# Kernel optimization log

Hardware: AMD Instinct MI355X
Metric: run time of the kernel (lower is better)

Reference implementation:

```python
import jax, jax.numpy as jnp
import numpy as np

N_NODES = 500000
N_EDGES = 1000000
H = 128


def setup_inputs() -> dict:
    key = jax.random.key(0)
    ks = jax.random.split(key, 8)
    s = 1.0 / np.sqrt(H)
    return {
        "z": jax.random.normal(ks[0], (N_NODES, H), dtype=jnp.float32),
        "w1": jax.random.normal(ks[1], (H, H), dtype=jnp.float32) * s,
        "b1": jax.random.normal(ks[2], (H,), dtype=jnp.float32) * s,
        "w2": jax.random.normal(ks[3], (H, H), dtype=jnp.float32) * s,
        "b2": jax.random.normal(ks[4], (H,), dtype=jnp.float32) * s,
        "wb": jax.random.normal(ks[5], (1, H, H), dtype=jnp.float32) * s,
        "bb": jax.random.normal(ks[6], (1,), dtype=jnp.float32) * s,
        "pot_arcs": jax.random.randint(ks[7], (N_EDGES, 2), 0, N_NODES, dtype=jnp.int64),
    }


def reference(z, w1, b1, w2, b2, wb, bb, pot_arcs):
    # Gather head/dep node embeddings per candidate arc: [E, H]
    x1 = z[pot_arcs[:, 0]]
    x2 = z[pot_arcs[:, 1]]
    # Per-node linear + relu (dropout is identity in eval mode)
    h1 = jax.nn.relu(x1 @ w1.T + b1)
    h2 = jax.nn.relu(x2 @ w2.T + b2)
    # Bilinear score: h1 @ W @ h2^T per edge, out_features=1
    score = jnp.einsum("eh,hk,ek->e", h1, wb[0], h2) + bb[0]
    return score
```

## Files before the change

kernel.cpp:

```cpp
#include <hip/hip_runtime.h>
#include <hip/hip_bf16.h>

#define HDIM 128

typedef short bf16x8 __attribute__((ext_vector_type(8)));
typedef short bf16x4 __attribute__((ext_vector_type(4)));
typedef unsigned short u16x8 __attribute__((ext_vector_type(8)));
typedef float f32x4 __attribute__((ext_vector_type(4)));

__device__ __forceinline__ short f2bf(float f) {
    __hip_bfloat16 h = __float2bfloat16(f);
    union { __hip_bfloat16 h; short s; } c; c.h = h; return c.s;
}
__device__ __forceinline__ float bf2f(unsigned short h) {
    union { unsigned u; float f; } c; c.u = ((unsigned)h) << 16; return c.f;
}
__device__ __forceinline__ bf16x8 pack8(float4 a, float4 b) {
    bf16x8 r;
    r[0] = f2bf(a.x); r[1] = f2bf(a.y); r[2] = f2bf(a.z); r[3] = f2bf(a.w);
    r[4] = f2bf(b.x); r[5] = f2bf(b.y); r[6] = f2bf(b.z); r[7] = f2bf(b.w);
    return r;
}

__device__ __forceinline__ void barrier_lds() {
    asm volatile("s_waitcnt lgkmcnt(0)" ::: "memory");
    __builtin_amdgcn_s_barrier();
    __builtin_amdgcn_sched_barrier(0);
}

__global__ __launch_bounds__(512, 4)
void node_phase(const float* __restrict__ z,
                const float* __restrict__ w1, const float* __restrict__ b1,
                const float* __restrict__ w2, const float* __restrict__ b2,
                const float* __restrict__ wb,
                unsigned short* __restrict__ g1, unsigned short* __restrict__ h2o,
                int N)
{
    __shared__ short zbb[32 * 128];
    __shared__ short h1x[32 * 128];
    __shared__ short h2x[32 * 128];
    __shared__ short g1x[32 * 128];

    const int t = threadIdx.x;
    const int lane = t & 63, wid = t >> 6;
    const int l15 = lane & 15, kgrp = lane >> 4;
    const int feat = wid * 16 + l15;

    bf16x8 w1f[4], w2f[4], wbf[4];
    {
        const float* w1r = w1 + (size_t)feat * HDIM;
        const float* w2r = w2 + (size_t)feat * HDIM;
#pragma unroll
        for (int kt = 0; kt < 4; ++kt) {
            int k0 = kt * 32 + kgrp * 8;
            w1f[kt] = pack8(*(const float4*)(w1r + k0), *(const float4*)(w1r + k0 + 4));
            w2f[kt] = pack8(*(const float4*)(w2r + k0), *(const float4*)(w2r + k0 + 4));
            bf16x8 r;
#pragma unroll
            for (int i = 0; i < 8; ++i) r[i] = f2bf(wb[(size_t)(k0 + i) * HDIM + feat]);
            wbf[kt] = r;
        }
    }
    f32x4 bias1, bias2;
#pragma unroll
    for (int r = 0; r < 4; ++r) {
        bias1[r] = b1[wid * 16 + kgrp * 4 + r];
        bias2[r] = b2[wid * 16 + kgrp * 4 + r];
    }

    const int srow = t >> 4;
    const int sp   = t & 15;
    const int sg   = sp ^ (srow & 7);

    const int ntiles = N >> 5;

    int tile = blockIdx.x;
    if (tile < ntiles) {
        const float* src = z + (size_t)(tile * 32 + srow) * HDIM + sg * 8;
        bf16x8 v = pack8(*(const float4*)src, *(const float4*)(src + 4));
        *(bf16x8*)&zbb[t * 8] = v;
    }
    __syncthreads();

    int prevbase = -1;
    for (; tile < ntiles; tile += gridDim.x) {
        const int base = tile * 32;
        const int nxtile = tile + (int)gridDim.x;
        const bool havenext = nxtile < ntiles;

        float4 zn0, zn1;
        if (havenext) {
            const float* src = z + (size_t)(nxtile * 32 + srow) * HDIM + sg * 8;
            zn0 = *(const float4*)src;
            zn1 = *(const float4*)(src + 4);
        }
        if (prevbase >= 0) {
            u16x8 vv = *(const u16x8*)&g1x[srow * 128 + sp * 8];
            *(u16x8*)&g1[(size_t)(prevbase + srow) * HDIM + (sp ^ (srow & 7)) * 8] = vv;
        }

#pragma unroll
        for (int gp = 0; gp < 2; ++gp) {
            const int m = gp * 16 + l15;
            bf16x8 zf[4];
#pragma unroll
            for (int kt = 0; kt < 4; ++kt) {
                int pos = (kt * 4 + kgrp) ^ (m & 7);
                zf[kt] = *(const bf16x8*)&zbb[m * 128 + pos * 8];
            }
            f32x4 a1 = bias1, a3 = bias2;
#pragma unroll
            for (int kt = 0; kt < 4; ++kt) {
                a1 = __builtin_amdgcn_mfma_f32_16x16x32_bf16(w1f[kt], zf[kt], a1, 0, 0, 0);
                a3 = __builtin_amdgcn_mfma_f32_16x16x32_bf16(w2f[kt], zf[kt], a3, 0, 0, 0);
            }
            const int ng = wid * 2 + (kgrp >> 1);
            const int sidx = m * 128 + ((ng ^ (m & 7)) << 3) + ((kgrp & 1) << 2);
            bf16x4 h1v, h2v;
#pragma unroll
            for (int r = 0; r < 4; ++r) {
                float x1 = a1[r] > 0.f ? a1[r] : 0.f;
                float x2 = a3[r] > 0.f ? a3[r] : 0.f;
                h1v[r] = f2bf(x1);
                h2v[r] = f2bf(x2);
            }
            *(bf16x4*)&h1x[sidx] = h1v;
            *(bf16x4*)&h2x[sidx] = h2v;
        }
        barrier_lds();

#pragma unroll
        for (int gp = 0; gp < 2; ++gp) {
            const int m = gp * 16 + l15;
            f32x4 ag = (f32x4){0.f, 0.f, 0.f, 0.f};
#pragma unroll
            for (int kt = 0; kt < 4; ++kt) {
                int pos = (kt * 4 + kgrp) ^ (m & 7);
                bf16x8 bf = *(const bf16x8*)&h1x[m * 128 + pos * 8];
                ag = __builtin_amdgcn_mfma_f32_16x16x32_bf16(wbf[kt], bf, ag, 0, 0, 0);
            }
            const int ng = wid * 2 + (kgrp >> 1);
            const int sidx = m * 128 + ((ng ^ (m & 7)) << 3) + ((kgrp & 1) << 2);
            bf16x4 gv;
#pragma unroll
            for (int r = 0; r < 4; ++r) gv[r] = f2bf(ag[r]);
            *(bf16x4*)&g1x[sidx] = gv;
        }
        {
            u16x8 vv = *(const u16x8*)&h2x[srow * 128 + sp * 8];
            *(u16x8*)&h2o[(size_t)(base + srow) * HDIM + (sp ^ (srow & 7)) * 8] = vv;
        }
        if (havenext) {
            *(bf16x8*)&zbb[t * 8] = pack8(zn0, zn1);
        }
        prevbase = base;
        barrier_lds();
    }

    if (prevbase >= 0) {
        u16x8 vv = *(const u16x8*)&g1x[srow * 128 + sp * 8];
        *(u16x8*)&g1[(size_t)(prevbase + srow) * HDIM + (sp ^ (srow & 7)) * 8] = vv;
    }
}

__global__ void detect_idx64(const int* __restrict__ arcs, int* __restrict__ flag)
{
    if (threadIdx.x == 0) {
        int is64 = 1;
        for (int j = 0; j < 64; ++j)
            if (arcs[2 * j + 1] != 0) { is64 = 0; break; }
        *flag = is64;
    }
}

__global__ __launch_bounds__(256, 8)
void edge_phase(const unsigned short* __restrict__ g1,
                const unsigned short* __restrict__ h2,
                const void* __restrict__ arcs,
                const int* __restrict__ flag,
                const float* __restrict__ bb,
                float* __restrict__ out, int E)
{
    const int t = threadIdx.x;
    const int sub = t & 15;
    const int e = blockIdx.x * 16 + (t >> 4);
    const int ec = e < E ? e : (E - 1);

    long long u, v;
    if (*flag) {
        const long long* a = (const long long*)arcs;
        u = a[2 * (size_t)ec]; v = a[2 * (size_t)ec + 1];
    } else {
        const int* a = (const int*)arcs;
        u = a[2 * (size_t)ec]; v = a[2 * (size_t)ec + 1];
    }

    u16x8 av = *(const u16x8*)(g1 + (size_t)u * HDIM + sub * 8);
    u16x8 bv = *(const u16x8*)(h2 + (size_t)v * HDIM + sub * 8);
    float s = 0.f;
#pragma unroll
    for (int i = 0; i < 8; ++i) s += bf2f(av[i]) * bf2f(bv[i]);

    s += __shfl_xor(s, 8, 16);
    s += __shfl_xor(s, 4, 16);
    s += __shfl_xor(s, 2, 16);
    s += __shfl_xor(s, 1, 16);

    if (sub == 0 && e < E) out[e] = s + bb[0];
}

extern "C" void kernel_launch(void* const* d_in, const int* in_sizes, int n_in,
                              void* d_out, int out_size, void* d_ws, size_t ws_size,
                              hipStream_t stream)
{
    const float* z  = (const float*)d_in[0];
    const float* w1 = (const float*)d_in[1];
    const float* b1 = (const float*)d_in[2];
    const float* w2 = (const float*)d_in[3];
    const float* b2 = (const float*)d_in[4];
    const float* wb = (const float*)d_in[5];
    const float* bb = (const float*)d_in[6];
    const void*  arcs = d_in[7];

    const int N = in_sizes[0] / HDIM;
    const int E = in_sizes[7] / 2;

    char* ws = (char*)d_ws;
    int* flag = (int*)ws;
    unsigned short* g1 = (unsigned short*)(ws + 256);
    unsigned short* h2 = g1 + (size_t)N * HDIM;

    detect_idx64<<<1, 64, 0, stream>>>((const int*)arcs, flag);

    node_phase<<<512, 512, 0, stream>>>(z, w1, b1, w2, b2, wb, g1, h2, N);

    int eblk = (E + 15) / 16;
    edge_phase<<<eblk, 256, 0, stream>>>(g1, h2, arcs, flag, bb, (float*)d_out, E);
}
```

Before: 190.5 us.

## Software-pipeline node phase across three tile stages with double-buffered LDS

Restructures the node kernel loop into a three-stage software pipeline: tile i does the W1/W2 MFMA stage, tile i-1 does the bilinear Wb stage, and tile i-2 has its g1 output written back. All LDS tiles are double-buffered so each iteration needs only one barrier instead of two. It also handles a partial final tile by clamping z reads and guarding stores. LDS use doubles to 64KB per block, which may cut how many blocks fit on a CU.

```diff
diff --git a/kernel.cpp b/kernel.cpp
--- a/kernel.cpp
+++ b/kernel.cpp
@@ -36,10 +36,10 @@
                 unsigned short* __restrict__ g1, unsigned short* __restrict__ h2o,
                 int N)
 {
-    __shared__ short zbb[32 * 128];
-    __shared__ short h1x[32 * 128];
-    __shared__ short h2x[32 * 128];
-    __shared__ short g1x[32 * 128];
+    __shared__ short zbb[2][4096];
+    __shared__ short h1x[2][4096];
+    __shared__ short h2x[2][4096];
+    __shared__ short g1x[2][4096];
 
     const int t = threadIdx.x;
     const int lane = t & 63, wid = t >> 6;
@@ -72,94 +72,97 @@
     const int sp   = t & 15;
     const int sg   = sp ^ (srow & 7);
 
-    const int ntiles = N >> 5;
-
-    int tile = blockIdx.x;
-    if (tile < ntiles) {
-        const float* src = z + (size_t)(tile * 32 + srow) * HDIM + sg * 8;
-        bf16x8 v = pack8(*(const float4*)src, *(const float4*)(src + 4));
-        *(bf16x8*)&zbb[t * 8] = v;
+    const int ntiles = (N + 31) >> 5;
+    const int myTiles = (ntiles > (int)blockIdx.x)
+                      ? ((ntiles - 1 - (int)blockIdx.x) / (int)gridDim.x + 1) : 0;
+    const int nit = myTiles + 2;
+    const int ng = wid * 2 + (kgrp >> 1);
+
+    if (myTiles > 0) {
+        int row = (int)blockIdx.x * 32 + srow;
+        int rc = row < N ? row : N - 1;
+        const float* src = z + (size_t)rc * HDIM + sg * 8;
+        *(bf16x8*)&zbb[0][t * 8] = pack8(*(const float4*)src, *(const float4*)(src + 4));
     }
     __syncthreads();
 
-    int prevbase = -1;
-    for (; tile < ntiles; tile += gridDim.x) {
-        const int base = tile * 32;
-        const int nxtile = tile + (int)gridDim.x;
-        const bool havenext = nxtile < ntiles;
+    for (int i = 0; i < nit; ++i) {
+        const int cur = i & 1, prv = cur ^ 1;
+        const int tvA = (int)blockIdx.x + i * (int)gridDim.x;
+        const bool vA = (i < myTiles);
+        const bool vB = (i >= 1) && (i - 1 < myTiles);
+        const bool vG = (i >= 2) && (i - 2 < myTiles);
+        const bool vP = (i + 1 < myTiles);
 
         float4 zn0, zn1;
-        if (havenext) {
-            const float* src = z + (size_t)(nxtile * 32 + srow) * HDIM + sg * 8;
+        if (vP) {
+            int row = (tvA + (int)gridDim.x) * 32 + srow;
+            int rc = row < N ? row : N - 1;
+            const float* src = z + (size_t)rc * HDIM + sg * 8;
             zn0 = *(const float4*)src;
             zn1 = *(const float4*)(src + 4);
         }
-        if (prevbase >= 0) {
-            u16x8 vv = *(const u16x8*)&g1x[srow * 128 + sp * 8];
-            *(u16x8*)&g1[(size_t)(prevbase + srow) * HDIM + (sp ^ (srow & 7)) * 8] = vv;
-        }
-
-#pragma unroll
-        for (int gp = 0; gp < 2; ++gp) {
-            const int m = gp * 16 + l15;
-            bf16x8 zf[4];
-#pragma unroll
-            for (int kt = 0; kt < 4; ++kt) {
-                int pos = (kt * 4 + kgrp) ^ (m & 7);
-                zf[kt] = *(const bf16x8*)&zbb[m * 128 + pos * 8];
+        if (vG) {
+            int row = (tvA - 2 * (int)gridDim.x) * 32 + srow;
+            u16x8 vv = *(const u16x8*)&g1x[prv][srow * 128 + sp * 8];
+            if (row < N) *(u16x8*)&g1[(size_t)row * HDIM + (sp ^ (srow & 7)) * 8] = vv;
+        }
+        if (vB) {
+            int row = (tvA - (int)gridDim.x) * 32 + srow;
+            u16x8 vv = *(const u16x8*)&h2x[prv][srow * 128 + sp * 8];
+            if (row < N) *(u16x8*)&h2o[(size_t)row * HDIM + (sp ^ (srow & 7)) * 8] = vv;
+        }
+        if (vA) {
+#pragma unroll
+            for (int gp = 0; gp < 2; ++gp) {
+                const int m = gp * 16 + l15;
+                bf16x8 zf[4];
+#pragma unroll
+                for (int kt = 0; kt < 4; ++kt) {
+                    int pos = (kt * 4 + kgrp) ^ (m & 7);
+                    zf[kt] = *(const bf16x8*)&zbb[cur][m * 128 + pos * 8];
+                }
+                f32x4 a1 = bias1, a3 = bias2;
+#pragma unroll
+                for (int kt = 0; kt < 4; ++kt) {
+                    a1 = __builtin_amdgcn_mfma_f32_16x16x32_bf16(w1f[kt], zf[kt], a1, 0, 0, 0);
+                    a3 = __builtin_amdgcn_mfma_f32_16x16x32_bf16(w2f[kt], zf[kt], a3, 0, 0, 0);
+                }
+                const int sidx = m * 128 + ((ng ^ (m & 7)) << 3) + ((kgrp & 1) << 2);
+                bf16x4 h1v, h2v;
+#pragma unroll
+                for (int r = 0; r < 4; ++r) {
+                    float x1 = a1[r] > 0.f ? a1[r] : 0.f;
+                    float x2 = a3[r] > 0.f ? a3[r] : 0.f;
+                    h1v[r] = f2bf(x1);
+                    h2v[r] = f2bf(x2);
+                }
+                *(bf16x4*)&h1x[cur][sidx] = h1v;
+                *(bf16x4*)&h2x[cur][sidx] = h2v;
             }
-            f32x4 a1 = bias1, a3 = bias2;
-#pragma unroll
-            for (int kt = 0; kt < 4; ++kt) {
-                a1 = __builtin_amdgcn_mfma_f32_16x16x32_bf16(w1f[kt], zf[kt], a1, 0, 0, 0);
-                a3 = __builtin_amdgcn_mfma_f32_16x16x32_bf16(w2f[kt], zf[kt], a3, 0, 0, 0);
+        }
+        if (vB) {
+#pragma unroll
+            for (int gp = 0; gp < 2; ++gp) {
+                const int m = gp * 16 + l15;
+                f32x4 ag = (f32x4){0.f, 0.f, 0.f, 0.f};
+#pragma unroll
+                for (int kt = 0; kt < 4; ++kt) {
+                    int pos = (kt * 4 + kgrp) ^ (m & 7);
+                    bf16x8 bf = *(const bf16x8*)&h1x[prv][m * 128 + pos * 8];
+                    ag = __builtin_amdgcn_mfma_f32_16x16x32_bf16(wbf[kt], bf, ag, 0, 0, 0);
+                }
+                const int sidx = m * 128 + ((ng ^ (m & 7)) << 3) + ((kgrp & 1) << 2);
+                bf16x4 gv;
+#pragma unroll
+                for (int r = 0; r < 4; ++r) gv[r] = f2bf(ag[r]);
+                *(bf16x4*)&g1x[cur][sidx] = gv;
             }
-            const int ng = wid * 2 + (kgrp >> 1);
-            const int sidx = m * 128 + ((ng ^ (m & 7)) << 3) + ((kgrp & 1) << 2);
-            bf16x4 h1v, h2v;
-#pragma unroll
-            for (int r = 0; r < 4; ++r) {
-                float x1 = a1[r] > 0.f ? a1[r] : 0.f;
-                float x2 = a3[r] > 0.f ? a3[r] : 0.f;
-                h1v[r] = f2bf(x1);
-                h2v[r] = f2bf(x2);
-            }
-            *(bf16x4*)&h1x[sidx] = h1v;
-            *(bf16x4*)&h2x[sidx] = h2v;
+        }
+        if (vP) {
+            *(bf16x8*)&zbb[prv][t * 8] = pack8(zn0, zn1);
         }
         barrier_lds();
-
-#pragma unroll
-        for (int gp = 0; gp < 2; ++gp) {
-            const int m = gp * 16 + l15;
-            f32x4 ag = (f32x4){0.f, 0.f, 0.f, 0.f};
-#pragma unroll
-            for (int kt = 0; kt < 4; ++kt) {
-                int pos = (kt * 4 + kgrp) ^ (m & 7);
-                bf16x8 bf = *(const bf16x8*)&h1x[m * 128 + pos * 8];
-                ag = __builtin_amdgcn_mfma_f32_16x16x32_bf16(wbf[kt], bf, ag, 0, 0, 0);
-            }
-            const int ng = wid * 2 + (kgrp >> 1);
-            const int sidx = m * 128 + ((ng ^ (m & 7)) << 3) + ((kgrp & 1) << 2);
-            bf16x4 gv;
-#pragma unroll
-            for (int r = 0; r < 4; ++r) gv[r] = f2bf(ag[r]);
-            *(bf16x4*)&g1x[sidx] = gv;
-        }
-        {
-            u16x8 vv = *(const u16x8*)&h2x[srow * 128 + sp * 8];
-            *(u16x8*)&h2o[(size_t)(base + srow) * HDIM + (sp ^ (srow & 7)) * 8] = vv;
-        }
-        if (havenext) {
-            *(bf16x8*)&zbb[t * 8] = pack8(zn0, zn1);
-        }
-        prevbase = base;
-        barrier_lds();
-    }
-
-    if (prevbase >= 0) {
-        u16x8 vv = *(const u16x8*)&g1x[srow * 128 + sp * 8];
-        *(u16x8*)&g1[(size_t)(prevbase + srow) * HDIM + (sp ^ (srow & 7)) * 8] = vv;
     }
 }
 
```

New measurement: 186.9 us. About the same (-1.9%).
